# Kernel tuning notes

Hardware: AMD Instinct MI355X
Metric: run time of the kernel (lower is better)

The kernel has to match this reference:

```python
import jax, jax.numpy as jnp
import numpy as np
from itertools import product

D = 128        # input voxel grid side
N_IN = 150000  # active input voxels
C_IN = 32
C_OUT = 64
M = 100000     # active output voxels kept after stride-2 downsample
EPS = 1e-5


def _build_rulebooks():
    rng = np.random.default_rng(0)
    flat = rng.choice(D ** 3, size=N_IN, replace=False)
    coords = np.stack(np.unravel_index(flat, (D, D, D)), axis=1).astype(np.int64)  # [N_IN,3]
    # SparseConv3d(kernel=2, stride=2, padding=1): input i contributes to output o with
    # i = 2*o - 1 + k, k in {0,1}; per dim exactly one k is valid -> o = (i+1)//2.
    out_all = (coords + 1) // 2
    koff = (coords + 1) % 2
    kidx = koff[:, 0] * 4 + koff[:, 1] * 2 + koff[:, 2]
    out_coords, inv = np.unique(out_all, axis=0, return_inverse=True)
    assert len(out_coords) >= M, 'not enough occupied parent voxels'
    out_coords = out_coords[:M]
    nbr_down = -np.ones((M, 8), np.int32)
    sel = inv < M
    nbr_down[inv[sel], kidx[sel]] = np.arange(N_IN, dtype=np.int32)[sel]
    # SubMConv3d(kernel=3, padding=1): output sites == input sites; neighbor table per offset.
    S = 67  # hash stride (out coords in [0,65), +1 shift keeps neighbor keys in range)
    key = (out_coords[:, 0] + 1) * S * S + (out_coords[:, 1] + 1) * S + (out_coords[:, 2] + 1)
    lut = -np.ones(S ** 3, np.int32)
    lut[key] = np.arange(M, dtype=np.int32)
    nbr_sub = np.empty((M, 27), np.int32)
    for k, (dx, dy, dz) in enumerate(product((-1, 0, 1), repeat=3)):
        nbr_sub[:, k] = lut[key + dx * S * S + dy * S + dz]
    return nbr_down, nbr_sub


def setup_inputs() -> dict:
    nbr_down, nbr_sub = _build_rulebooks()
    key = jax.random.key(0)
    k0, k1, k2, k3, k4 = jax.random.split(key, 5)
    ones = jnp.ones((C_OUT,), jnp.float32)
    zeros = jnp.zeros((C_OUT,), jnp.float32)
    return {
        'x_feats': jax.random.normal(k0, (N_IN, C_IN), jnp.float32),
        'w_down': jax.random.normal(k1, (8, C_IN, C_OUT), jnp.float32) / np.sqrt(8 * C_IN),
        'g_down': ones, 'b_down': zeros,
        'w_proj': jax.random.normal(k2, (C_OUT, C_OUT), jnp.float32) / np.sqrt(C_OUT),
        'g_p': ones, 'b_p': zeros,
        'w1': jax.random.normal(k3, (27, C_OUT, C_OUT), jnp.float32) / np.sqrt(27 * C_OUT),
        'g1': ones, 'b1': zeros,
        'w2': jax.random.normal(k4, (27, C_OUT, C_OUT), jnp.float32) / np.sqrt(27 * C_OUT),
        'g2': ones, 'b2': zeros,
        'nbr_down': jnp.asarray(nbr_down),
        'nbr_sub': jnp.asarray(nbr_sub),
    }


def _bn(f, g, b):
    # BatchNorm1d in training mode over the active-voxel dim (biased variance)
    m = f.mean(0)
    v = jnp.mean((f - m) ** 2, 0)
    return (f - m) * jax.lax.rsqrt(v + EPS) * g + b


def _spconv(feats, nbr, W):
    # rulebook gather-GEMM-scatter: out[m] = sum_k feats[nbr[m,k]] @ W[k]  (nbr=-1 -> zero)
    n = feats.shape[0]
    fpad = jnp.concatenate([feats, jnp.zeros((1, feats.shape[1]), feats.dtype)], axis=0)
    idx = jnp.where(nbr < 0, n, nbr)
    out = jnp.zeros((nbr.shape[0], W.shape[2]), feats.dtype)
    for k in range(W.shape[0]):  # fixed small kernel volume (8 or 27)
        out = out + fpad[idx[:, k]] @ W[k]
    return out


def reference(x_feats, w_down, g_down, b_down, w_proj, g_p, b_p,
              w1, g1, b1, w2, g2, b2, nbr_down, nbr_sub):
    # DonwBlock.down: SparseConv3d -> BN -> ReLU
    x = jax.nn.relu(_bn(_spconv(x_feats, nbr_down, w_down), g_down, b_down))
    # DoubleConv.proj: 1x1 SubMConv (plain linear on features) -> BN
    res = _bn(x @ w_proj, g_p, b_p)
    # conv1 -> bn1 -> relu -> conv2 -> bn2 -> +proj -> relu
    out = jax.nn.relu(_bn(_spconv(x, nbr_sub, w1), g1, b1))
    out = _bn(_spconv(out, nbr_sub, w2), g2, b2) + res
    return jax.nn.relu(out)
```

## Files before the change

kernel.cpp:

```cpp
#include <hip/hip_runtime.h>

static constexpr int M_ROWS = 100000;
static constexpr int N_IN   = 150000;
static constexpr int C_IN   = 32;
static constexpr int CO     = 64;
static constexpr float EPS  = 1e-5f;

typedef __bf16 bf16x8 __attribute__((ext_vector_type(8)));
typedef float  f32x4  __attribute__((ext_vector_type(4)));
typedef unsigned short u16x8 __attribute__((ext_vector_type(8)));
typedef short  short8 __attribute__((ext_vector_type(8)));
typedef unsigned int u32;

static __device__ __forceinline__ unsigned short f2bf(float f) {
    unsigned int u = __builtin_bit_cast(unsigned int, f);
    u += 0x7fff + ((u >> 16) & 1);
    return (unsigned short)(u >> 16);
}
static __device__ __forceinline__ float bf2f(unsigned short h) {
    unsigned int u = ((unsigned int)h) << 16;
    return __builtin_bit_cast(float, u);
}

static __device__ __forceinline__ void gload_lds16(const void* g, void* l) {
    __builtin_amdgcn_global_load_lds(
        (const __attribute__((address_space(1))) u32*)g,
        (__attribute__((address_space(3))) u32*)l, 16, 0, 0);
}

__global__ __launch_bounds__(256) void cvt_bf16(
    const float* __restrict__ in, unsigned short* __restrict__ out, int n8)
{
    int i = blockIdx.x * 256 + threadIdx.x;
    if (i >= n8) return;
    float4 a = ((const float4*)in)[2 * i];
    float4 b = ((const float4*)in)[2 * i + 1];
    u16x8 v;
    v[0] = f2bf(a.x); v[1] = f2bf(a.y); v[2] = f2bf(a.z); v[3] = f2bf(a.w);
    v[4] = f2bf(b.x); v[5] = f2bf(b.y); v[6] = f2bf(b.z); v[7] = f2bf(b.w);
    ((u16x8*)out)[i] = v;
}

__global__ __launch_bounds__(256) void wt_cvt_all(
    const float* __restrict__ wd, const float* __restrict__ wp,
    const float* __restrict__ w1, const float* __restrict__ w2,
    unsigned short* __restrict__ wdT, unsigned short* __restrict__ wpT,
    unsigned short* __restrict__ w1T, unsigned short* __restrict__ w2T)
{
    int t = blockIdx.x * 256 + threadIdx.x;
    if (t >= 241664) return;
    const float* W; unsigned short* WT; int cin, tt;
    if (t < 16384)       { W = wd; WT = wdT; cin = 32; tt = t; }
    else if (t < 20480)  { W = wp; WT = wpT; cin = 64; tt = t - 16384; }
    else if (t < 131072) { W = w1; WT = w1T; cin = 64; tt = t - 20480; }
    else                 { W = w2; WT = w2T; cin = 64; tt = t - 131072; }
    int k  = tt / (cin * 64);
    int r  = tt - k * (cin * 64);
    int ci = r >> 6;
    int co = r & 63;
    int xm = (cin == 64) ? ((co & 7) << 4) : ((co & 3) << 4);
    int phys = co * (cin * 2) + ((ci * 2) ^ xm);
    WT[(size_t)k * cin * 64 + (phys >> 1)] = f2bf(W[tt]);
}

template<int CIN, int KOFF, bool GATHER, bool OUTBF>
__global__ __launch_bounds__(512) void spconv_mfma(
    const unsigned short* __restrict__ fB,
    int nZero,
    const int*   __restrict__ nbr,
    const unsigned short* __restrict__ WTs,
    void* __restrict__ outp,
    float* __restrict__ part)
{
    constexpr int KS     = CIN / 32;
    constexpr int ST     = 2;
    constexpr int ROWS   = 256;
    constexpr int SLAB   = CIN * 64;
    constexpr int SWAVES = CIN / 8;

    __shared__ unsigned short Wl[2][SLAB];
    __shared__ int nbrS[GATHER ? ROWS * KOFF : 4];
    __shared__ float red[8][2][64];

    const int tid  = threadIdx.x;
    const int lane = tid & 63;
    const int wv   = tid >> 6;
    const int colb = lane & 15;
    const int kgrp = lane >> 4;

    const int nwg = gridDim.x;
    const int q   = nwg >> 3, r8 = nwg & 7;
    const int xcd = blockIdx.x & 7, pos = blockIdx.x >> 3;
    const int wg  = (xcd < r8 ? xcd * (q + 1) : r8 * (q + 1) + (xcd - r8) * q) + pos;
    const int m0  = wg * ROWS;

    auto stageW = [&](int k, int b) {
        if (wv < SWAVES) {
            const unsigned short* gp = WTs + (size_t)k * SLAB + wv * 512 + lane * 8;
            void* lp = &Wl[b][wv * 512];
            gload_lds16(gp, lp);
        }
    };

    stageW(0, 0);
    if (GATHER) {
        const int* src = nbr + (size_t)m0 * KOFF;
        constexpr int TOT = ROWS * KOFF;
        if (m0 + ROWS <= M_ROWS) {
            #pragma unroll 1
            for (int i = tid; i < TOT / 4; i += 512)
                ((int4*)nbrS)[i] = ((const int4*)src)[i];
        } else {
            #pragma unroll 1
            for (int i = tid; i < TOT; i += 512) {
                int r = i / KOFF;
                nbrS[i] = (m0 + r < M_ROWS) ? src[i] : -1;
            }
        }
    }
    __syncthreads();

    auto gatherA = [&](int k, bf16x8 (&dst)[ST][KS]) {
        #pragma unroll
        for (int st = 0; st < ST; ++st) {
            int rloc = wv * (ST * 16) + st * 16 + colb;
            int idx;
            if (GATHER) idx = nbrS[rloc * KOFF + k];
            else        idx = (m0 + rloc < M_ROWS) ? (m0 + rloc) : -1;
            if (idx < 0) idx = nZero;
            const unsigned short* fp = fB + (size_t)idx * CIN + kgrp * 8;
            #pragma unroll
            for (int s = 0; s < KS; ++s)
                dst[st][s] = *reinterpret_cast<const bf16x8*>(fp + s * 32);
        }
    };

    f32x4 acc[ST][4] = {};

    auto compute = [&](int buf, const bf16x8 (&a)[ST][KS]) {
        bf16x8 w[4][KS];
        const char* base = (const char*)&Wl[0][0] + (size_t)buf * SLAB * 2;
        #pragma unroll
        for (int n = 0; n < 4; ++n) {
            int r  = n * 16 + colb;
            int xm = (CIN == 64) ? ((r & 7) << 4) : ((r & 3) << 4);
            #pragma unroll
            for (int s = 0; s < KS; ++s) {
                int c2 = kgrp * 16 + s * 64;
                int phys = r * (CIN * 2) + (c2 ^ xm);
                w[n][s] = *reinterpret_cast<const bf16x8*>(base + phys);
            }
        }
        #pragma unroll
        for (int st = 0; st < ST; ++st)
            #pragma unroll
            for (int n = 0; n < 4; ++n)
                #pragma unroll
                for (int s = 0; s < KS; ++s)
                    acc[st][n] = __builtin_amdgcn_mfma_f32_16x16x32_bf16(
                        a[st][s], w[n][s], acc[st][n], 0, 0, 0);
    };

    #pragma unroll 1
    for (int k = 0; k < KOFF; ++k) {
        bf16x8 a[ST][KS];
        gatherA(k, a);
        if (k + 1 < KOFF) stageW(k + 1, (k + 1) & 1);
        compute(k & 1, a);
        if (k + 1 < KOFF) __syncthreads();
    }

    #pragma unroll
    for (int st = 0; st < ST; ++st) {
        int rbase = m0 + wv * (ST * 16) + st * 16 + kgrp * 4;
        #pragma unroll
        for (int j = 0; j < 4; ++j) {
            int row = rbase + j;
            if (row < M_ROWS) {
                if (OUTBF) {
                    unsigned short* o = (unsigned short*)outp;
                    #pragma unroll
                    for (int n = 0; n < 4; ++n)
                        o[(size_t)row * 64 + n * 16 + colb] = f2bf(acc[st][n][j]);
                } else {
                    float* o = (float*)outp;
                    #pragma unroll
                    for (int n = 0; n < 4; ++n)
                        o[(size_t)row * 64 + n * 16 + colb] = acc[st][n][j];
                }
            }
        }
    }

    float s4[4], q4[4];
    #pragma unroll
    for (int n = 0; n < 4; ++n) {
        float s = 0.f, qq = 0.f;
        #pragma unroll
        for (int st = 0; st < ST; ++st)
            #pragma unroll
            for (int j = 0; j < 4; ++j) {
                float v = acc[st][n][j];
                s += v; qq += v * v;
            }
        s4[n] = s; q4[n] = qq;
    }
    #pragma unroll
    for (int n = 0; n < 4; ++n) {
        s4[n] += __shfl_xor(s4[n], 16); s4[n] += __shfl_xor(s4[n], 32);
        q4[n] += __shfl_xor(q4[n], 16); q4[n] += __shfl_xor(q4[n], 32);
    }
    if (kgrp == 0) {
        #pragma unroll
        for (int n = 0; n < 4; ++n) {
            red[wv][0][n * 16 + colb] = s4[n];
            red[wv][1][n * 16 + colb] = q4[n];
        }
    }
    __syncthreads();
    if (tid < 64) {
        float S = 0.f, Q = 0.f;
        #pragma unroll
        for (int w8 = 0; w8 < 8; ++w8) { S += red[w8][0][tid]; Q += red[w8][1][tid]; }
        part[(size_t)wg * 128 + tid]      = S;
        part[(size_t)wg * 128 + 64 + tid] = Q;
    }
}

__global__ __launch_bounds__(1024) void bn_finalize(
    const float* __restrict__ part, int nblocks,
    const float* __restrict__ gg, const float* __restrict__ bb,
    float* __restrict__ ss, int M)
{
    const int tid = threadIdx.x;
    const int c   = tid & 63;
    const int grp = tid >> 6;
    float S = 0.f, Q = 0.f;
    int i = grp;
    for (; i + 48 < nblocks; i += 64) {
        float a0 = part[(size_t)(i     ) * 128 + c];
        float a1 = part[(size_t)(i + 16) * 128 + c];
        float a2 = part[(size_t)(i + 32) * 128 + c];
        float a3 = part[(size_t)(i + 48) * 128 + c];
        float q0 = part[(size_t)(i     ) * 128 + 64 + c];
        float q1 = part[(size_t)(i + 16) * 128 + 64 + c];
        float q2 = part[(size_t)(i + 32) * 128 + 64 + c];
        float q3 = part[(size_t)(i + 48) * 128 + 64 + c];
        S += a0 + a1 + a2 + a3;
        Q += q0 + q1 + q2 + q3;
    }
    for (; i < nblocks; i += 16) {
        S += part[(size_t)i * 128 + c];
        Q += part[(size_t)i * 128 + 64 + c];
    }
    __shared__ float sh[2][16][64];
    sh[0][grp][c] = S; sh[1][grp][c] = Q;
    __syncthreads();
    if (tid < 64) {
        float Sa = 0.f, Qa = 0.f;
        #pragma unroll
        for (int j = 0; j < 16; ++j) { Sa += sh[0][j][tid]; Qa += sh[1][j][tid]; }
        float mean = Sa / (float)M;
        float var  = Qa / (float)M - mean * mean;
        float rstd = rsqrtf(var + EPS);
        float sc = gg[tid] * rstd;
        ss[tid]      = sc;
        ss[64 + tid] = bb[tid] - mean * sc;
    }
}

template<bool INBF, bool BF16OUT, bool RES, bool RELU>
__global__ __launch_bounds__(256) void bn_apply(
    const void* __restrict__ yp, const float* __restrict__ ss,
    const unsigned short* __restrict__ res, void* __restrict__ out, int n8)
{
    for (int i = blockIdx.x * 256 + threadIdx.x; i < n8; i += gridDim.x * 256) {
        float v[8];
        if (INBF) {
            u16x8 u = ((const u16x8*)yp)[i];
            #pragma unroll
            for (int j = 0; j < 8; ++j) v[j] = bf2f(u[j]);
        } else {
            float4 a = ((const float4*)yp)[2 * i];
            float4 b = ((const float4*)yp)[2 * i + 1];
            v[0] = a.x; v[1] = a.y; v[2] = a.z; v[3] = a.w;
            v[4] = b.x; v[5] = b.y; v[6] = b.z; v[7] = b.w;
        }
        int c0 = (i * 8) & 63;
        #pragma unroll
        for (int j = 0; j < 8; ++j)
            v[j] = v[j] * ss[c0 + j] + ss[64 + c0 + j];
        if (RES) {
            u16x8 rv = ((const u16x8*)res)[i];
            #pragma unroll
            for (int j = 0; j < 8; ++j) v[j] += bf2f(rv[j]);
        }
        if (RELU) {
            #pragma unroll
            for (int j = 0; j < 8; ++j) v[j] = fmaxf(v[j], 0.f);
        }
        if (BF16OUT) {
            u16x8 o;
            #pragma unroll
            for (int j = 0; j < 8; ++j) o[j] = f2bf(v[j]);
            ((u16x8*)out)[i] = o;
        } else {
            float4 oa, ob;
            oa.x = v[0]; oa.y = v[1]; oa.z = v[2]; oa.w = v[3];
            ob.x = v[4]; ob.y = v[5]; ob.z = v[6]; ob.w = v[7];
            ((float4*)out)[2 * i]     = oa;
            ((float4*)out)[2 * i + 1] = ob;
        }
    }
}

extern "C" void kernel_launch(void* const* d_in, const int* in_sizes, int n_in,
                              void* d_out, int out_size, void* d_ws, size_t ws_size,
                              hipStream_t stream)
{
    const float* x_feats = (const float*)d_in[0];
    const float* w_down  = (const float*)d_in[1];
    const float* g_down  = (const float*)d_in[2];
    const float* b_down  = (const float*)d_in[3];
    const float* w_proj  = (const float*)d_in[4];
    const float* g_p     = (const float*)d_in[5];
    const float* b_p     = (const float*)d_in[6];
    const float* w1      = (const float*)d_in[7];
    const float* g1      = (const float*)d_in[8];
    const float* b1      = (const float*)d_in[9];
    const float* w2      = (const float*)d_in[10];
    const float* g2      = (const float*)d_in[11];
    const float* b2      = (const float*)d_in[12];
    const int*   nbr_down = (const int*)d_in[13];
    const int*   nbr_sub  = (const int*)d_in[14];
    float* out = (float*)d_out;

    const int M = M_ROWS;
    const int conv_grid = (M + 255) / 256;
    const size_t feat2 = (size_t)(M + 1) * CO * 2;
    auto align = [](size_t x) { return (x + 255) & ~(size_t)255; };

    char* ws = (char*)d_ws;
    size_t off = 0;
    unsigned short* xin16 = (unsigned short*)(ws + off); off += align((size_t)(N_IN + 1) * C_IN * 2);
    unsigned short* wdT   = (unsigned short*)(ws + off); off += align((size_t)8 * CO * C_IN * 2);
    unsigned short* wpT   = (unsigned short*)(ws + off); off += align((size_t)1 * CO * CO * 2);
    unsigned short* w1T   = (unsigned short*)(ws + off); off += align((size_t)27 * CO * CO * 2);
    unsigned short* w2T   = (unsigned short*)(ws + off); off += align((size_t)27 * CO * CO * 2);
    unsigned short* Yb    = (unsigned short*)(ws + off); off += align(feat2);
    unsigned short* bufRb = (unsigned short*)(ws + off); off += align(feat2);
    unsigned short* xB    = (unsigned short*)(ws + off); off += align(feat2);
    unsigned short* zB    = (unsigned short*)(ws + off); off += align(feat2);
    float* part = (float*)(ws + off); off += align((size_t)1024 * 128 * 4);
    float* ss0  = (float*)(ws + off);
    float* ss1  = ss0 + 128;
    float* ss2  = ss1 + 128;
    float* ss3  = ss2 + 128;

    const int n8 = M * CO / 8;
    const int ew_grid = 2048;

    hipMemsetAsync(xin16 + (size_t)N_IN * C_IN, 0, C_IN * 2, stream);
    hipMemsetAsync(xB + (size_t)M * CO, 0, CO * 2, stream);
    hipMemsetAsync(zB + (size_t)M * CO, 0, CO * 2, stream);

    {
        int nf8 = N_IN * C_IN / 8;
        cvt_bf16<<<(nf8 + 255) / 256, 256, 0, stream>>>(x_feats, xin16, nf8);
        wt_cvt_all<<<(241664 + 255) / 256, 256, 0, stream>>>(
            w_down, w_proj, w1, w2, wdT, wpT, w1T, w2T);
    }

    spconv_mfma<C_IN, 8, true, true><<<conv_grid, 512, 0, stream>>>(
        xin16, N_IN, nbr_down, wdT, Yb, part);
    bn_finalize<<<1, 1024, 0, stream>>>(part, conv_grid, g_down, b_down, ss0, M);
    bn_apply<true, true, false, true><<<ew_grid, 256, 0, stream>>>(Yb, ss0, nullptr, xB, n8);

    spconv_mfma<CO, 1, false, true><<<conv_grid, 512, 0, stream>>>(
        xB, M, nullptr, wpT, Yb, part);
    bn_finalize<<<1, 1024, 0, stream>>>(part, conv_grid, g_p, b_p, ss1, M);
    bn_apply<true, true, false, false><<<ew_grid, 256, 0, stream>>>(Yb, ss1, nullptr, bufRb, n8);

    spconv_mfma<CO, 27, true, true><<<conv_grid, 512, 0, stream>>>(
        xB, M, nbr_sub, w1T, Yb, part);
    bn_finalize<<<1, 1024, 0, stream>>>(part, conv_grid, g1, b1, ss2, M);
    bn_apply<true, true, false, true><<<ew_grid, 256, 0, stream>>>(Yb, ss2, nullptr, zB, n8);

    spconv_mfma<CO, 27, true, true><<<conv_grid, 512, 0, stream>>>(
        zB, M, nbr_sub, w2T, Yb, part);
    bn_finalize<<<1, 1024, 0, stream>>>(part, conv_grid, g2, b2, ss3, M);
    bn_apply<true, false, true, true><<<ew_grid, 256, 0, stream>>>(Yb, ss3, bufRb, out, n8);
}
```

Measured before the change: 171.7 us.

## Fuse down-BN/ReLU into projection GEMM and defer projection BN to final apply

Adds a kernel that applies the down-conv BN+ReLU on the fly, writes the activated bf16 features, and runs the 1x1 projection MFMA with BN statistics in one pass. This replaces one bn_apply, the projection conv launch and the projection bn_apply. The projection BN affine is now applied inside the final bn_apply via a second scale/shift table. The result is two fewer launches and fewer full-tensor read/write passes, but the residual is stored as raw bf16 before normalization, which may change rounding slightly.

```diff
diff --git a/kernel.cpp b/kernel.cpp
--- a/kernel.cpp
+++ b/kernel.cpp
@@ -20,6 +20,10 @@
 static __device__ __forceinline__ float bf2f(unsigned short h) {
     unsigned int u = ((unsigned int)h) << 16;
     return __builtin_bit_cast(float, u);
+}
+static __device__ __forceinline__ bf16x8 bfzero() {
+    short8 z = {0,0,0,0,0,0,0,0};
+    return __builtin_bit_cast(bf16x8, z);
 }
 
 static __device__ __forceinline__ void gload_lds16(const void* g, void* l) {
@@ -222,6 +226,144 @@
         float S = 0.f, Q = 0.f;
         #pragma unroll
         for (int w8 = 0; w8 < 8; ++w8) { S += red[w8][0][tid]; Q += red[w8][1][tid]; }
+        part[(size_t)wg * 128 + tid]      = S;
+        part[(size_t)wg * 128 + 64 + tid] = Q;
+    }
+}
+
+__global__ __launch_bounds__(256) void bn_proj_fused(
+    const unsigned short* __restrict__ Yb,
+    const float* __restrict__ ss,
+    const unsigned short* __restrict__ wpT,
+    unsigned short* __restrict__ xB,
+    unsigned short* __restrict__ prOut,
+    float* __restrict__ part)
+{
+    constexpr int SLAB = 64 * 64;
+
+    __shared__ unsigned short Wl[SLAB];
+    __shared__ float red[4][2][64];
+
+    const int tid  = threadIdx.x;
+    const int lane = tid & 63;
+    const int wv   = tid >> 6;
+    const int colb = lane & 15;
+    const int kgrp = lane >> 4;
+
+    const int nwg = gridDim.x;
+    const int q   = nwg >> 3, r8 = nwg & 7;
+    const int xcd = blockIdx.x & 7, pos = blockIdx.x >> 3;
+    const int wg  = (xcd < r8 ? xcd * (q + 1) : r8 * (q + 1) + (xcd - r8) * q) + pos;
+    const int m0  = wg * 256;
+
+    #pragma unroll
+    for (int r = 0; r < 2; ++r) {
+        const void* gp = wpT + (size_t)(r * 256 + tid) * 8;
+        void* lp = &Wl[(size_t)(r * 256 + wv * 64) * 8];
+        gload_lds16(gp, lp);
+    }
+
+    float sc[2][8], sh[2][8];
+    #pragma unroll
+    for (int s = 0; s < 2; ++s) {
+        int c0 = kgrp * 8 + s * 32;
+        float4 A = *(const float4*)(ss + c0);
+        float4 B = *(const float4*)(ss + c0 + 4);
+        float4 C = *(const float4*)(ss + 64 + c0);
+        float4 D = *(const float4*)(ss + 64 + c0 + 4);
+        sc[s][0]=A.x; sc[s][1]=A.y; sc[s][2]=A.z; sc[s][3]=A.w;
+        sc[s][4]=B.x; sc[s][5]=B.y; sc[s][6]=B.z; sc[s][7]=B.w;
+        sh[s][0]=C.x; sh[s][1]=C.y; sh[s][2]=C.z; sh[s][3]=C.w;
+        sh[s][4]=D.x; sh[s][5]=D.y; sh[s][6]=D.z; sh[s][7]=D.w;
+    }
+    __syncthreads();
+
+    f32x4 acc[4][4] = {};
+
+    #pragma unroll
+    for (int st = 0; st < 4; ++st) {
+        bf16x8 a[2];
+        int row = m0 + wv * 64 + st * 16 + colb;
+        if (row < M_ROWS) {
+            const unsigned short* fp = Yb + (size_t)row * 64 + kgrp * 8;
+            #pragma unroll
+            for (int s = 0; s < 2; ++s) {
+                u16x8 u = *reinterpret_cast<const u16x8*>(fp + s * 32);
+                u16x8 o;
+                #pragma unroll
+                for (int j = 0; j < 8; ++j) {
+                    float v = bf2f(u[j]) * sc[s][j] + sh[s][j];
+                    v = fmaxf(v, 0.f);
+                    o[j] = f2bf(v);
+                }
+                a[s] = __builtin_bit_cast(bf16x8, o);
+                *reinterpret_cast<u16x8*>(xB + (size_t)row * 64 + kgrp * 8 + s * 32) = o;
+            }
+        } else {
+            a[0] = bfzero(); a[1] = bfzero();
+        }
+        bf16x8 w[4][2];
+        #pragma unroll
+        for (int n = 0; n < 4; ++n) {
+            int r  = n * 16 + colb;
+            int xm = (r & 7) << 4;
+            #pragma unroll
+            for (int s = 0; s < 2; ++s) {
+                int phys = r * 128 + ((kgrp * 16 + s * 64) ^ xm);
+                w[n][s] = *reinterpret_cast<const bf16x8*>((const char*)&Wl[0] + phys);
+            }
+        }
+        #pragma unroll
+        for (int n = 0; n < 4; ++n)
+            #pragma unroll
+            for (int s = 0; s < 2; ++s)
+                acc[st][n] = __builtin_amdgcn_mfma_f32_16x16x32_bf16(
+                    a[s], w[n][s], acc[st][n], 0, 0, 0);
+    }
+
+    #pragma unroll
+    for (int st = 0; st < 4; ++st) {
+        int rbase = m0 + wv * 64 + st * 16 + kgrp * 4;
+        #pragma unroll
+        for (int j = 0; j < 4; ++j) {
+            int row = rbase + j;
+            if (row < M_ROWS) {
+                #pragma unroll
+                for (int n = 0; n < 4; ++n)
+                    prOut[(size_t)row * 64 + n * 16 + colb] = f2bf(acc[st][n][j]);
+            }
+        }
+    }
+
+    float s4[4], q4[4];
+    #pragma unroll
+    for (int n = 0; n < 4; ++n) {
+        float s = 0.f, qq = 0.f;
+        #pragma unroll
+        for (int st = 0; st < 4; ++st)
+            #pragma unroll
+            for (int j = 0; j < 4; ++j) {
+                float v = acc[st][n][j];
+                s += v; qq += v * v;
+            }
+        s4[n] = s; q4[n] = qq;
+    }
+    #pragma unroll
+    for (int n = 0; n < 4; ++n) {
+        s4[n] += __shfl_xor(s4[n], 16); s4[n] += __shfl_xor(s4[n], 32);
+        q4[n] += __shfl_xor(q4[n], 16); q4[n] += __shfl_xor(q4[n], 32);
+    }
+    if (kgrp == 0) {
+        #pragma unroll
+        for (int n = 0; n < 4; ++n) {
+            red[wv][0][n * 16 + colb] = s4[n];
+            red[wv][1][n * 16 + colb] = q4[n];
+        }
+    }
+    __syncthreads();
+    if (tid < 64) {
+        float S = red[0][0][tid] + red[1][0][tid] + red[2][0][tid] + red[3][0][tid];
+        float Q = red[0][1][tid] + red[1][1][tid] + red[2][1][tid] + red[3][1][tid];
         part[(size_t)wg * 128 + tid]      = S;
         part[(size_t)wg * 128 + 64 + tid] = Q;
     }
@@ -272,7 +414,8 @@
 template<bool INBF, bool BF16OUT, bool RES, bool RELU>
 __global__ __launch_bounds__(256) void bn_apply(
     const void* __restrict__ yp, const float* __restrict__ ss,
-    const unsigned short* __restrict__ res, void* __restrict__ out, int n8)
+    const unsigned short* __restrict__ res, const float* __restrict__ ssr,
+    void* __restrict__ out, int n8)
 {
     for (int i = blockIdx.x * 256 + threadIdx.x; i < n8; i += gridDim.x * 256) {
         float v[8];
@@ -293,7 +436,8 @@
         if (RES) {
             u16x8 rv = ((const u16x8*)res)[i];
             #pragma unroll
-            for (int j = 0; j < 8; ++j) v[j] += bf2f(rv[j]);
+            for (int j = 0; j < 8; ++j)
+                v[j] += bf2f(rv[j]) * ssr[c0 + j] + ssr[64 + c0 + j];
         }
         if (RELU) {
             #pragma unroll
@@ -374,20 +518,19 @@
     spconv_mfma<C_IN, 8, true, true><<<conv_grid, 512, 0, stream>>>(
         xin16, N_IN, nbr_down, wdT, Yb, part);
     bn_finalize<<<1, 1024, 0, stream>>>(part, conv_grid, g_down, b_down, ss0, M);
-    bn_apply<true, true, false, true><<<ew_grid, 256, 0, stream>>>(Yb, ss0, nullptr, xB, n8);
-
-    spconv_mfma<CO, 1, false, true><<<conv_grid, 512, 0, stream>>>(
-        xB, M, nullptr, wpT, Yb, part);
+
+    bn_proj_fused<<<conv_grid, 256, 0, stream>>>(Yb, ss0, wpT, xB, bufRb, part);
     bn_finalize<<<1, 1024, 0, stream>>>(part, conv_grid, g_p, b_p, ss1, M);
-    bn_apply<true, true, false, false><<<ew_grid, 256, 0, stream>>>(Yb, ss1, nullptr, bufRb, n8);
 
     spconv_mfma<CO, 27, true, true><<<conv_grid, 512, 0, stream>>>(
         xB, M, nbr_sub, w1T, Yb, part);
     bn_finalize<<<1, 1024, 0, stream>>>(part, conv_grid, g1, b1, ss2, M);
-    bn_apply<true, true, false, true><<<ew_grid, 256, 0, stream>>>(Yb, ss2, nullptr, zB, n8);
+    bn_apply<true, true, false, true><<<ew_grid, 256, 0, stream>>>(
+        Yb, ss2, nullptr, nullptr, zB, n8);
 
     spconv_mfma<CO, 27, true, true><<<conv_grid, 512, 0, stream>>>(
         zB, M, nbr_sub, w2T, Yb, part);
     bn_finalize<<<1, 1024, 0, stream>>>(part, conv_grid, g2, b2, ss3, M);
-    bn_apply<true, false, true, true><<<ew_grid, 256, 0, stream>>>(Yb, ss3, bufRb, out, n8);
-}
+    bn_apply<true, false, true, true><<<ew_grid, 256, 0, stream>>>(
+        Yb, ss3, bufRb, ss1, out, n8);
+}
```

Measured after the change: 158.7 us. 7.5% less time.
